# Kernel tuning notes

Measured on AMD Instinct MI355X. Metric: run time of the kernel, lower is better.

## Reference

```python
import jax, jax.numpy as jnp
import numpy as np
import math

N = 40000
E = 1280000
HID = 128
NF = 128
NG = 50
L = 3
CUTOFF = 10.0


def ssp(x):
    # shifted softplus: softplus(x) - log(2)
    return jax.nn.softplus(x) - jnp.float32(math.log(2.0))


def setup_inputs() -> dict:
    key = jax.random.key(0)
    ks = jax.random.split(key, 16)
    z = jax.random.randint(ks[0], (N,), 0, 100)
    pos = jax.random.normal(ks[1], (N, 3), dtype=jnp.float32) * 3.0
    batch = jnp.zeros((N,), dtype=jnp.int32)
    edge_index = jax.random.randint(ks[2], (2, E), 0, N)
    s = 0.1
    emb = jax.random.normal(ks[3], (100, HID), dtype=jnp.float32) * s
    mlp_w1 = jax.random.normal(ks[4], (L, NG, NF), dtype=jnp.float32) * s
    mlp_b1 = jnp.zeros((L, NF), dtype=jnp.float32)
    mlp_w2 = jax.random.normal(ks[5], (L, NF, NF), dtype=jnp.float32) * s
    mlp_b2 = jnp.zeros((L, NF), dtype=jnp.float32)
    conv_w1 = jax.random.normal(ks[6], (L, HID, NF), dtype=jnp.float32) * s  # no bias
    conv_w2 = jax.random.normal(ks[7], (L, NF, HID), dtype=jnp.float32) * s
    conv_b2 = jnp.zeros((L, HID), dtype=jnp.float32)
    lin_w = jax.random.normal(ks[8], (L, HID, HID), dtype=jnp.float32) * s
    lin_b = jnp.zeros((L, HID), dtype=jnp.float32)
    lin1_w = jax.random.normal(ks[9], (HID, HID // 2), dtype=jnp.float32) * s
    lin1_b = jnp.zeros((HID // 2,), dtype=jnp.float32)
    return {
        "z": z, "pos": pos, "batch": batch, "edge_index": edge_index,
        "emb": emb, "mlp_w1": mlp_w1, "mlp_b1": mlp_b1, "mlp_w2": mlp_w2,
        "mlp_b2": mlp_b2, "conv_w1": conv_w1, "conv_w2": conv_w2,
        "conv_b2": conv_b2, "lin_w": lin_w, "lin_b": lin_b,
        "lin1_w": lin1_w, "lin1_b": lin1_b,
    }


def reference(z, pos, batch, edge_index, emb, mlp_w1, mlp_b1, mlp_w2, mlp_b2,
              conv_w1, conv_w2, conv_b2, lin_w, lin_b, lin1_w, lin1_b):
    n = z.shape[0]
    row, col = edge_index[0], edge_index[1]
    # edge distances (radius-graph edge weights)
    diff = pos[row] - pos[col]                       # [E,3]
    edge_weight = jnp.sqrt(jnp.sum(diff * diff, axis=-1))  # [E]
    # Gaussian smearing
    offset = jnp.linspace(0.0, CUTOFF, NG, dtype=jnp.float32)
    coeff = -0.5 / (offset[1] - offset[0]) ** 2
    edge_attr = jnp.exp(coeff * (edge_weight[:, None] - offset[None, :]) ** 2)  # [E,NG]
    # cosine cutoff
    C = 0.5 * (jnp.cos(edge_weight * (jnp.pi / CUTOFF)) + 1.0)  # [E]

    h = emb[z]  # [N,HID]
    for l in range(L):
        W = ssp(edge_attr @ mlp_w1[l] + mlp_b1[l]) @ mlp_w2[l] + mlp_b2[l]  # [E,NF]
        W = W * C[:, None]
        x = h @ conv_w1[l]                      # [N,NF]
        msg = x[row] * W                        # gather + filter, [E,NF]
        agg = jax.ops.segment_sum(msg, col, num_segments=n)  # scatter-add, [N,NF]
        x = agg @ conv_w2[l] + conv_b2[l]       # [N,HID]
        x = ssp(x)
        x = x @ lin_w[l] + lin_b[l]
        h = h + x
    return ssp(h @ lin1_w + lin1_b)  # [N,HID//2]
```

## Files before the change

### kernel.cpp

```cpp
#include <hip/hip_runtime.h>
#include <math.h>


typedef _Float16 f16;
typedef _Float16 half8 __attribute__((ext_vector_type(8)));
typedef _Float16 half4v __attribute__((ext_vector_type(4)));
typedef float f32x4 __attribute__((ext_vector_type(4)));

#define NGAUSS 50
#define HIDF   128
#define NBINS  8192
#define DMAXF  40.0f
#define NLAYER 3
#define XST    132
#define BSHIFT 9
#define MAXBUCK 128
#define SCAP  20480

static __device__ __forceinline__ float sspf(float v) {
    return fmaxf(v, 0.0f) + log1pf(expf(-fabsf(v))) - 0.6931471805599453f;
}

__global__ __launch_bounds__(256) void k_stage(const int* __restrict__ ei,
                                               const float* __restrict__ pos,
                                               int* __restrict__ scnt,
                                               uint2* __restrict__ staging,
                                               int E, int nbuck) {
    const float SCALE = (float)(NBINS - 1) / DMAXF;
    __shared__ int bhist[MAXBUCK];
    __shared__ int boff[MAXBUCK];
    __shared__ int gpos[MAXBUCK];
    __shared__ uint2 recs[4096];
    __shared__ unsigned char lbuck[4096];
    int t = threadIdx.x;
    for (int i = t; i < nbuck; i += 256) bhist[i] = 0;
    __syncthreads();
    int e0 = blockIdx.x * 4096;
    int cnt_here = min(4096, E - e0);
    unsigned pay[16];
    unsigned short cc[16];
    short rk[16];
#pragma unroll
    for (int k = 0; k < 16; ++k) {
        int idx = t + k * 256;
        rk[k] = -1;
        if (idx < cnt_here) {
            int e = e0 + idx;
            int r = ei[e], c = ei[E + e];
            float dx = pos[3*r+0] - pos[3*c+0];
            float dy = pos[3*r+1] - pos[3*c+1];
            float dz = pos[3*r+2] - pos[3*c+2];
            float d = sqrtf(dx*dx + dy*dy + dz*dz);
            float u = fminf(d * SCALE, (float)(NBINS - 1));
            int i0 = min((int)u, NBINS - 2);
            float w0 = u - (float)i0;
            int wq = (int)(w0 * 8.0f + 0.5f);
            if (wq == 8) { i0 = min(i0 + 1, NBINS - 2); wq = 0; }
            pay[k] = ((unsigned)i0 << 19) | ((unsigned)wq << 16) | (unsigned)r;
            cc[k] = (unsigned short)c;
            rk[k] = (short)atomicAdd(&bhist[c >> BSHIFT], 1);
        }
    }
    __syncthreads();
    if (t == 0) {
        int run = 0;
        for (int b = 0; b < nbuck; ++b) { boff[b] = run; run += bhist[b]; }
    }
    __syncthreads();
    if (t < nbuck) gpos[t] = atomicAdd(&scnt[t], bhist[t]);
    __syncthreads();
#pragma unroll
    for (int k = 0; k < 16; ++k) {
        if (rk[k] >= 0) {
            int b = cc[k] >> BSHIFT;
            int slot = boff[b] + rk[k];
            recs[slot] = make_uint2(pay[k], (unsigned)cc[k]);
            lbuck[slot] = (unsigned char)b;
        }
    }
    __syncthreads();
    for (int i = t; i < cnt_here; i += 256) {
        int b = lbuck[i];
        staging[(size_t)b * SCAP + gpos[b] + (i - boff[b])] = recs[i];
    }
}

__global__ __launch_bounds__(1024) void k_place(const uint2* __restrict__ staging,
                                                const int* __restrict__ scnt,
                                                int* __restrict__ meta,
                                                int* __restrict__ offs,
                                                int n, int nbuck) {
    __shared__ int lcnt[512], loff[512], lcur[512];
    __shared__ int ldsm[SCAP];
    __shared__ int ebase_s;
    int b = blockIdx.x, t = threadIdx.x;
    int cntb = scnt[b];
    if (t == 0) {
        int run = 0;
        for (int j = 0; j < b; ++j) run += scnt[j];
        ebase_s = run;
    }
    for (int j = t; j < 512; j += 1024) { lcnt[j] = 0; lcur[j] = 0; }
    __syncthreads();
    int ebase = ebase_s;
    const uint2* sb = staging + (size_t)b * SCAP;
    for (int i = t; i < cntb; i += 1024)
        atomicAdd(&lcnt[sb[i].y & 511], 1);
    __syncthreads();
    if (t < 512) loff[t] = lcnt[t];
    __syncthreads();
    for (int o = 1; o < 512; o <<= 1) {
        int v = 0;
        if (t < 512) { v = loff[t]; if (t >= o) v += loff[t - o]; }
        __syncthreads();
        if (t < 512) loff[t] = v;
        __syncthreads();
    }
    int nb0 = b << BSHIFT;
    if (t < 512) {
        int node = nb0 + t;
        if (node < n) offs[node] = ebase + loff[t] - lcnt[t];
    }
    if (b == nbuck - 1 && t == 0) offs[n] = ebase + cntb;
    __syncthreads();
    for (int i = t; i < cntb; i += 1024) {
        uint2 r = sb[i];
        int cl = (int)(r.y & 511);
        int lpos = (loff[cl] - lcnt[cl]) + atomicAdd(&lcur[cl], 1);
        if (lpos < SCAP) ldsm[lpos] = (int)r.x;
        else meta[ebase + lpos] = (int)r.x;
    }
    __syncthreads();
    int lim = min(cntb, SCAP);
    for (int i = t; i < lim; i += 1024) meta[ebase + i] = ldsm[i];
}

__global__ __launch_bounds__(128) void k_table(const float* __restrict__ w1,
                                               const float* __restrict__ b1,
                                               const float* __restrict__ w2,
                                               const float* __restrict__ b2,
                                               f16* __restrict__ T) {
    const float DELTA = 10.0f / 49.0f;
    const float COEFF = -0.5f / (DELTA * DELTA);
    const float HSTEP = DMAXF / (float)(NBINS - 1);
    __shared__ float ea[8][NGAUSS];
    __shared__ float u[8][HIDF];
    int l = blockIdx.y, b0 = blockIdx.x * 8, j = threadIdx.x;
    for (int idx = j; idx < 8 * NGAUSS; idx += 128) {
        int bb = idx / NGAUSS, g = idx % NGAUSS;
        float d = (float)(b0 + bb) * HSTEP;
        float diff = d - (float)g * DELTA;
        ea[bb][g] = expf(COEFF * diff * diff);
    }
    __syncthreads();
    float acc[8];
    {
        float bias = b1[l * HIDF + j];
#pragma unroll
        for (int b = 0; b < 8; ++b) acc[b] = bias;
        const float* w1l = w1 + (size_t)l * NGAUSS * HIDF;
        for (int g = 0; g < NGAUSS; ++g) {
            float wv = w1l[g * HIDF + j];
#pragma unroll
            for (int b = 0; b < 8; ++b) acc[b] = fmaf(ea[b][g], wv, acc[b]);
        }
#pragma unroll
        for (int b = 0; b < 8; ++b) u[b][j] = sspf(acc[b]);
    }
    __syncthreads();
    {
        float bias = b2[l * HIDF + j];
#pragma unroll
        for (int b = 0; b < 8; ++b) acc[b] = bias;
        const float* w2l = w2 + (size_t)l * HIDF * HIDF;
        for (int k = 0; k < HIDF; ++k) {
            float wv = w2l[k * HIDF + j];
#pragma unroll
            for (int b = 0; b < 8; ++b) acc[b] = fmaf(u[b][k], wv, acc[b]);
        }
    }
    f16* Tl = T + ((size_t)l * NBINS + b0) * HIDF;
#pragma unroll
    for (int b = 0; b < 8; ++b) {
        float d = (float)(b0 + b) * HSTEP;
        float C = 0.5f * (cosf(d * (float)(M_PI / 10.0)) + 1.0f);
        Tl[b * HIDF + j] = (f16)(acc[b] * C);
    }
}

__global__ void k_wpack(const float* __restrict__ cw1, const float* __restrict__ cw2,
                        const float* __restrict__ lw, const float* __restrict__ l1w,
                        f16* __restrict__ Wp) {
    int mat = blockIdx.y;
    int N = (mat == 9) ? 64 : HIDF;
    int ntiles = N >> 4;
    int tid = blockIdx.x * 256 + threadIdx.x;
    int lane = tid & 63, ks = (tid >> 6) & 3, nt = tid >> 8;
    if (nt >= ntiles) return;
    const float* W;
    if (mat < 9) {
        int l = mat / 3, kind = mat % 3;
        W = (kind == 0 ? cw1 : kind == 1 ? cw2 : lw) + (size_t)l * HIDF * HIDF;
    } else {
        W = l1w;
    }
    int kbase = ks * 32 + (lane >> 4) * 8;
    int col = nt * 16 + (lane & 15);
    half8 st;
#pragma unroll
    for (int j = 0; j < 8; ++j) st[j] = (f16)W[(size_t)(kbase + j) * N + col];
    *(half8*)&Wp[(size_t)mat * 16384 + ((size_t)(nt * 4 + ks) * 64 + lane) * 8] = st;
}

#define AGG_EDGE(yy)                                                         \
    {                                                                        \
        int row_ = (yy) & 0xFFFF;                                            \
        int i0_ = ((unsigned)(yy)) >> 19;                                    \
        float w0_ = (float)(((yy) >> 16) & 7) * 0.125f;                      \
        half8 x0_ = *(const half8*)&xj[(size_t)row_ * HIDF];                 \
        half8 ta_ = *(const half8*)&Tj[(size_t)i0_ * HIDF];                  \
        half8 tb_ = *(const half8*)&Tj[(size_t)(i0_ + 1) * HIDF];            \
        _Pragma("unroll")                                                    \
        for (int j = 0; j < 8; ++j) {                                        \
            float t0 = (float)ta_[j];                                        \
            float f0 = fmaf(w0_, (float)tb_[j] - t0, t0);                    \
            a[j] = fmaf((float)x0_[j], f0, a[j]);                            \
        }                                                                    \
    }

__global__ __launch_bounds__(256) void k_agg(const f16* __restrict__ x,
                                             const f16* __restrict__ T,
                                             const int* __restrict__ meta,
                                             const int* __restrict__ offs,
                                             f16* __restrict__ agg, int n) {
    int node = (blockIdx.x * blockDim.x + threadIdx.x) >> 4;
    int lane = threadIdx.x & 15;
    if (node >= n) return;
    int beg = offs[node], end = offs[node + 1];
    const f16* xj = x + lane * 8;
    const f16* Tj = T + lane * 8;
    float a[8] = {};
    for (int chunk = beg; chunk < end; chunk += 16) {
        int cnt = min(16, end - chunk);
        int mm = meta[chunk + min(lane, cnt - 1)];
        int q = 0;
        for (; q + 4 <= cnt; q += 4) {
            int y0 = __shfl(mm, q + 0, 16);
            int y1 = __shfl(mm, q + 1, 16);
            int y2 = __shfl(mm, q + 2, 16);
            int y3 = __shfl(mm, q + 3, 16);
            AGG_EDGE(y0)
            AGG_EDGE(y1)
            AGG_EDGE(y2)
            AGG_EDGE(y3)
        }
        for (; q < cnt; ++q) {
            int y0 = __shfl(mm, q, 16);
            AGG_EDGE(y0)
        }
    }
    half8 st;
#pragma unroll
    for (int j = 0; j < 8; ++j) st[j] = (f16)a[j];
    *(half8*)&agg[(size_t)node * HIDF + lane * 8] = st;
}

__global__ __launch_bounds__(256) void k_init_gemm(const int* __restrict__ z,
                                                   const float* __restrict__ emb,
                                                   const f16* __restrict__ w1p,
                                                   f16* __restrict__ xout) {
    int lane = threadIdx.x & 63;
    int wid = threadIdx.x >> 6;
    int m0 = blockIdx.x * 64 + wid * 16;
    int mrow = lane & 15, quad = lane >> 4;
    const float* er = emb + (size_t)z[m0 + mrow] * HIDF + quad * 8;
    half8 afr[4];
#pragma unroll
    for (int ks = 0; ks < 4; ++ks) {
        float4 a = *(const float4*)(er + ks * 32);
        float4 b = *(const float4*)(er + ks * 32 + 4);
        half8 f = {(f16)a.x, (f16)a.y, (f16)a.z, (f16)a.w,
                   (f16)b.x, (f16)b.y, (f16)b.z, (f16)b.w};
        afr[ks] = f;
    }
    f32x4 acc[8];
#pragma unroll
    for (int t = 0; t < 8; ++t) acc[t] = (f32x4){0.f, 0.f, 0.f, 0.f};
    const f16* bp = w1p + (size_t)lane * 8;
#pragma unroll
    for (int t = 0; t < 8; ++t)
#pragma unroll
        for (int ks = 0; ks < 4; ++ks) {
            half8 bfr = *(const half8*)(bp + (size_t)(t * 4 + ks) * 512);
            acc[t] = __builtin_amdgcn_mfma_f32_16x16x32_f16(afr[ks], bfr, acc[t], 0, 0, 0);
        }
    int col0 = lane & 15;
    int growb = m0 + quad * 4;
#pragma unroll
    for (int t = 0; t < 8; ++t)
#pragma unroll
        for (int r = 0; r < 4; ++r)
            xout[(size_t)(growb + r) * HIDF + t * 16 + col0] = (f16)acc[t][r];
}

template <int NT3, bool LAYER0, bool WRITE_H>
__global__ __launch_bounds__(256) void k_fused(const f16* __restrict__ agg,
                                               const f16* __restrict__ w2p,
                                               const float* __restrict__ b2,
                                               const f16* __restrict__ lwp,
                                               const float* __restrict__ lb,
                                               const f16* __restrict__ b3p,
                                               const float* __restrict__ b3,
                                               float* __restrict__ hio,
                                               const int* __restrict__ z,
                                               const float* __restrict__ emb,
                                               f16* __restrict__ xout,
                                               float* __restrict__ fout) {
    __shared__ f16 Xs[4][16][XST];
    int lane = threadIdx.x & 63;
    int wid = threadIdx.x >> 6;
    int m0 = blockIdx.x * 64 + wid * 16;
    int mrow = lane & 15, quad = lane >> 4;
    int col0 = mrow;
    int growb = m0 + quad * 4;
    f16 (*X)[XST] = Xs[wid];

    half8 afr[4];
    {
        const f16* Ar = agg + (size_t)(m0 + mrow) * HIDF + quad * 8;
#pragma unroll
        for (int ks = 0; ks < 4; ++ks) afr[ks] = *(const half8*)(Ar + ks * 32);
    }
    f32x4 acc[8];
#pragma unroll
    for (int t = 0; t < 8; ++t) acc[t] = (f32x4){0.f, 0.f, 0.f, 0.f};
    {
        const f16* bp = w2p + (size_t)lane * 8;
#pragma unroll
        for (int t = 0; t < 8; ++t)
#pragma unroll
            for (int ks = 0; ks < 4; ++ks) {
                half8 bfr = *(const half8*)(bp + (size_t)(t * 4 + ks) * 512);
                acc[t] = __builtin_amdgcn_mfma_f32_16x16x32_f16(afr[ks], bfr, acc[t], 0, 0, 0);
            }
    }
#pragma unroll
    for (int t = 0; t < 8; ++t) {
        int col = t * 16 + col0;
        float bv = b2[col];
#pragma unroll
        for (int r = 0; r < 4; ++r)
            X[quad * 4 + r][col] = (f16)sspf(acc[t][r] + bv);
    }
#pragma unroll
    for (int ks = 0; ks < 4; ++ks) {
        half4v lo = *(const half4v*)&X[mrow][ks * 32 + quad * 8];
        half4v hi = *(const half4v*)&X[mrow][ks * 32 + quad * 8 + 4];
        half8 f;
#pragma unroll
        for (int j = 0; j < 4; ++j) { f[j] = lo[j]; f[4 + j] = hi[j]; }
        afr[ks] = f;
    }
#pragma unroll
    for (int t = 0; t < 8; ++t) acc[t] = (f32x4){0.f, 0.f, 0.f, 0.f};
    {
        const f16* bp = lwp + (size_t)lane * 8;
#pragma unroll
        for (int t = 0; t < 8; ++t)
#pragma unroll
            for (int ks = 0; ks < 4; ++ks) {
                half8 bfr = *(const half8*)(bp + (size_t)(t * 4 + ks) * 512);
                acc[t] = __builtin_amdgcn_mfma_f32_16x16x32_f16(afr[ks], bfr, acc[t], 0, 0, 0);
            }
    }
    int zr[4];
    if (LAYER0) {
#pragma unroll
        for (int r = 0; r < 4; ++r) zr[r] = z[growb + r];
    }
#pragma unroll
    for (int t = 0; t < 8; ++t) {
        int col = t * 16 + col0;
        float bv = lb[col];
#pragma unroll
        for (int r = 0; r < 4; ++r) {
            int grow = growb + r;
            float resid = LAYER0 ? emb[(size_t)zr[r] * HIDF + col]
                                 : hio[(size_t)grow * HIDF + col];
            float hp = acc[t][r] + bv + resid;
            if (WRITE_H) hio[(size_t)grow * HIDF + col] = hp;
            X[quad * 4 + r][col] = (f16)hp;
        }
    }
#pragma unroll
    for (int ks = 0; ks < 4; ++ks) {
        half4v lo = *(const half4v*)&X[mrow][ks * 32 + quad * 8];
        half4v hi = *(const half4v*)&X[mrow][ks * 32 + quad * 8 + 4];
        half8 f;
#pragma unroll
        for (int j = 0; j < 4; ++j) { f[j] = lo[j]; f[4 + j] = hi[j]; }
        afr[ks] = f;
    }
#pragma unroll
    for (int t = 0; t < NT3; ++t) acc[t] = (f32x4){0.f, 0.f, 0.f, 0.f};
    {
        const f16* bp = b3p + (size_t)lane * 8;
#pragma unroll
        for (int t = 0; t < NT3; ++t)
#pragma unroll
            for (int ks = 0; ks < 4; ++ks) {
                half8 bfr = *(const half8*)(bp + (size_t)(t * 4 + ks) * 512);
                acc[t] = __builtin_amdgcn_mfma_f32_16x16x32_f16(afr[ks], bfr, acc[t], 0, 0, 0);
            }
    }
    if (NT3 == 8) {
#pragma unroll
        for (int t = 0; t < 8; ++t)
#pragma unroll
            for (int r = 0; r < 4; ++r)
                xout[(size_t)(growb + r) * HIDF + t * 16 + col0] = (f16)acc[t][r];
    } else {
#pragma unroll
        for (int t = 0; t < NT3; ++t) {
            int col = t * 16 + col0;
            float bv = b3[col];
#pragma unroll
            for (int r = 0; r < 4; ++r)
                fout[(size_t)(growb + r) * (NT3 * 16) + col] = sspf(acc[t][r] + bv);
        }
    }
}

extern "C" void kernel_launch(void* const* d_in, const int* in_sizes, int n_in,
                              void* d_out, int out_size, void* d_ws, size_t ws_size,
                              hipStream_t stream) {
    const int*   z       = (const int*)d_in[0];
    const float* pos     = (const float*)d_in[1];
    const int*   ei      = (const int*)d_in[3];
    const float* emb     = (const float*)d_in[4];
    const float* mlp_w1  = (const float*)d_in[5];
    const float* mlp_b1  = (const float*)d_in[6];
    const float* mlp_w2  = (const float*)d_in[7];
    const float* mlp_b2  = (const float*)d_in[8];
    const float* conv_w1 = (const float*)d_in[9];
    const float* conv_w2 = (const float*)d_in[10];
    const float* conv_b2 = (const float*)d_in[11];
    const float* lin_w   = (const float*)d_in[12];
    const float* lin_b   = (const float*)d_in[13];
    const float* lin1_w  = (const float*)d_in[14];
    const float* lin1_b  = (const float*)d_in[15];
    float* out = (float*)d_out;

    int n = in_sizes[0];
    int E = in_sizes[3] / 2;
    int nbuck = (n + 511) >> 9;

    char* ws = (char*)d_ws;
    size_t off = 0;
    auto alloc = [&](size_t bytes) -> void* {
        void* p = ws + off;
        off = (off + bytes + 255) & ~(size_t)255;
        return p;
    };
    float* h     = (float*)alloc((size_t)n * HIDF * 4);
    f16*   x16   = (f16*)alloc((size_t)n * HIDF * 2);
    f16*   agg16 = (f16*)alloc((size_t)n * HIDF * 2);
    f16*   T16   = (f16*)alloc((size_t)NLAYER * NBINS * HIDF * 2);
    int*   meta  = (int*)alloc((size_t)E * 4);
    int*   offs  = (int*)alloc((size_t)(n + 1) * 4);
    int*   scnt  = (int*)alloc((size_t)nbuck * 4);
    uint2* staging = (uint2*)alloc((size_t)nbuck * SCAP * 8);
    f16*   Wp    = (f16*)alloc((size_t)10 * 16384 * 2);

    const int tb = 256;
    hipMemsetAsync(scnt, 0, (size_t)nbuck * 4, stream);
    hipLaunchKernelGGL(k_stage, dim3((E + 4095) / 4096), dim3(tb), 0, stream,
                       ei, pos, scnt, staging, E, nbuck);
    hipLaunchKernelGGL(k_place, dim3(nbuck), dim3(1024), 0, stream,
                       staging, scnt, meta, offs, n, nbuck);
    hipLaunchKernelGGL(k_wpack, dim3(8, 10), dim3(tb), 0, stream,
                       conv_w1, conv_w2, lin_w, lin1_w, Wp);
    hipLaunchKernelGGL(k_table, dim3(NBINS / 8, NLAYER), dim3(128), 0, stream,
                       mlp_w1, mlp_b1, mlp_w2, mlp_b2, T16);

    int gemmblocks = n / 64;
    int aggblocks = (n * 16 + tb - 1) / tb;
    hipLaunchKernelGGL(k_init_gemm, dim3(gemmblocks), dim3(tb), 0, stream,
                       z, emb, Wp + (size_t)0 * 16384, x16);
    hipLaunchKernelGGL(k_agg, dim3(aggblocks), dim3(tb), 0, stream,
                       x16, T16 + (size_t)0 * NBINS * HIDF, meta, offs, agg16, n);
    hipLaunchKernelGGL(HIP_KERNEL_NAME(k_fused<8, true, true>), dim3(gemmblocks), dim3(tb), 0, stream,
                       agg16, Wp + (size_t)1 * 16384, conv_b2 + 0 * HIDF,
                       Wp + (size_t)2 * 16384, lin_b + 0 * HIDF,
                       Wp + (size_t)3 * 16384, (const float*)nullptr,
                       h, z, emb, x16, (float*)nullptr);
    hipLaunchKernelGGL(k_agg, dim3(aggblocks), dim3(tb), 0, stream,
                       x16, T16 + (size_t)1 * NBINS * HIDF, meta, offs, agg16, n);
    hipLaunchKernelGGL(HIP_KERNEL_NAME(k_fused<8, false, true>), dim3(gemmblocks), dim3(tb), 0, stream,
                       agg16, Wp + (size_t)4 * 16384, conv_b2 + 1 * HIDF,
                       Wp + (size_t)5 * 16384, lin_b + 1 * HIDF,
                       Wp + (size_t)6 * 16384, (const float*)nullptr,
                       h, (const int*)nullptr, (const float*)nullptr, x16, (float*)nullptr);
    hipLaunchKernelGGL(k_agg, dim3(aggblocks), dim3(tb), 0, stream,
                       x16, T16 + (size_t)2 * NBINS * HIDF, meta, offs, agg16, n);
    hipLaunchKernelGGL(HIP_KERNEL_NAME(k_fused<4, false, false>), dim3(gemmblocks), dim3(tb), 0, stream,
                       agg16, Wp + (size_t)7 * 16384, conv_b2 + 2 * HIDF,
                       Wp + (size_t)8 * 16384, lin_b + 2 * HIDF,
                       Wp + (size_t)9 * 16384, lin1_b,
                       h, (const int*)nullptr, (const float*)nullptr, (f16*)nullptr, out);
    (void)n_in; (void)out_size; (void)ws_size;
}
```

Baseline: 439.2 us.

## Shrink CSR buckets, parallelize scans, use packed fp16 interpolation in aggregation

Bucket size for the counting-sort CSR build drops from 512 to 128 nodes, so there are more, smaller buckets and k_place runs more blocks with less LDS. The serial prefix sums over bucket counts in k_stage and k_place become wavefront shuffle scans. The aggregation kernel now does the filter-table interpolation with packed half8 arithmetic and uses nontemporal loads and stores for meta and agg. The fp16 interpolation lowers accuracy slightly, and the extra buckets increase global atomics on scnt.

Measured after the change: 471.8 us. +7.4%, slower.

```diff
diff --git a/kernel.cpp b/kernel.cpp
--- a/kernel.cpp
+++ b/kernel.cpp
@@ -13,9 +13,10 @@
 #define DMAXF  40.0f
 #define NLAYER 3
 #define XST    132
-#define BSHIFT 9
-#define MAXBUCK 128
-#define SCAP  20480
+#define BSHIFT 7
+#define NPB    128
+#define MAXBUCK 512
+#define SCAP  5120
 
 static __device__ __forceinline__ float sspf(float v) {
     return fmaxf(v, 0.0f) + log1pf(expf(-fabsf(v))) - 0.6931471805599453f;
@@ -31,9 +32,9 @@
     __shared__ int boff[MAXBUCK];
     __shared__ int gpos[MAXBUCK];
     __shared__ uint2 recs[4096];
-    __shared__ unsigned char lbuck[4096];
+    __shared__ unsigned short lbuck[4096];
     int t = threadIdx.x;
-    for (int i = t; i < nbuck; i += 256) bhist[i] = 0;
+    for (int i = t; i < MAXBUCK; i += 256) bhist[i] = 0;
     __syncthreads();
     int e0 = blockIdx.x * 4096;
     int cnt_here = min(4096, E - e0);
@@ -62,20 +63,30 @@
         }
     }
     __syncthreads();
-    if (t == 0) {
+    if (t < 64) {
+        int base = t * 8;
+        int s[8];
         int run = 0;
-        for (int b = 0; b < nbuck; ++b) { boff[b] = run; run += bhist[b]; }
-    }
-    __syncthreads();
-    if (t < nbuck) gpos[t] = atomicAdd(&scnt[t], bhist[t]);
-    __syncthreads();
+#pragma unroll
+        for (int j = 0; j < 8; ++j) { s[j] = run; run += bhist[base + j]; }
+        int incl = run;
+        for (int o = 1; o < 64; o <<= 1) {
+            int v = __shfl_up(incl, o, 64);
+            if (t >= o) incl += v;
+        }
+        int excl = incl - run;
+#pragma unroll
+        for (int j = 0; j < 8; ++j) boff[base + j] = excl + s[j];
+    }
+    __syncthreads();
+    for (int i = t; i < nbuck; i += 256) gpos[i] = atomicAdd(&scnt[i], bhist[i]);
 #pragma unroll
     for (int k = 0; k < 16; ++k) {
         if (rk[k] >= 0) {
             int b = cc[k] >> BSHIFT;
             int slot = boff[b] + rk[k];
             recs[slot] = make_uint2(pay[k], (unsigned)cc[k]);
-            lbuck[slot] = (unsigned char)b;
+            lbuck[slot] = (unsigned short)b;
         }
     }
     __syncthreads();
@@ -90,34 +101,39 @@
                                                 int* __restrict__ meta,
                                                 int* __restrict__ offs,
                                                 int n, int nbuck) {
-    __shared__ int lcnt[512], loff[512], lcur[512];
+    __shared__ int lcnt[NPB], loff[NPB], lcur[NPB];
     __shared__ int ldsm[SCAP];
+    __shared__ int wsum[16];
     __shared__ int ebase_s;
     int b = blockIdx.x, t = threadIdx.x;
     int cntb = scnt[b];
+    int part = 0;
+    for (int j = t; j < b; j += 1024) part += scnt[j];
+    for (int o = 32; o > 0; o >>= 1) part += __shfl_down(part, o, 64);
+    if ((t & 63) == 0) wsum[t >> 6] = part;
+    if (t < NPB) { lcnt[t] = 0; lcur[t] = 0; }
+    __syncthreads();
     if (t == 0) {
-        int run = 0;
-        for (int j = 0; j < b; ++j) run += scnt[j];
-        ebase_s = run;
-    }
-    for (int j = t; j < 512; j += 1024) { lcnt[j] = 0; lcur[j] = 0; }
-    __syncthreads();
-    int ebase = ebase_s;
+        int r = 0;
+        for (int w = 0; w < 16; ++w) r += wsum[w];
+        ebase_s = r;
+    }
     const uint2* sb = staging + (size_t)b * SCAP;
     for (int i = t; i < cntb; i += 1024)
-        atomicAdd(&lcnt[sb[i].y & 511], 1);
-    __syncthreads();
-    if (t < 512) loff[t] = lcnt[t];
-    __syncthreads();
-    for (int o = 1; o < 512; o <<= 1) {
+        atomicAdd(&lcnt[sb[i].y & (NPB - 1)], 1);
+    __syncthreads();
+    int ebase = ebase_s;
+    if (t < NPB) loff[t] = lcnt[t];
+    __syncthreads();
+    for (int o = 1; o < NPB; o <<= 1) {
         int v = 0;
-        if (t < 512) { v = loff[t]; if (t >= o) v += loff[t - o]; }
+        if (t < NPB) { v = loff[t]; if (t >= o) v += loff[t - o]; }
         __syncthreads();
-        if (t < 512) loff[t] = v;
+        if (t < NPB) loff[t] = v;
         __syncthreads();
     }
     int nb0 = b << BSHIFT;
-    if (t < 512) {
+    if (t < NPB) {
         int node = nb0 + t;
         if (node < n) offs[node] = ebase + loff[t] - lcnt[t];
     }
@@ -125,7 +141,7 @@
     __syncthreads();
     for (int i = t; i < cntb; i += 1024) {
         uint2 r = sb[i];
-        int cl = (int)(r.y & 511);
+        int cl = (int)(r.y & (NPB - 1));
         int lpos = (loff[cl] - lcnt[cl]) + atomicAdd(&lcur[cl], 1);
         if (lpos < SCAP) ldsm[lpos] = (int)r.x;
         else meta[ebase + lpos] = (int)r.x;
@@ -216,16 +232,17 @@
     {                                                                        \
         int row_ = (yy) & 0xFFFF;                                            \
         int i0_ = ((unsigned)(yy)) >> 19;                                    \
-        float w0_ = (float)(((yy) >> 16) & 7) * 0.125f;                      \
+        f16 w0h_ = (f16)((float)(((yy) >> 16) & 7) * 0.125f);                \
         half8 x0_ = *(const half8*)&xj[(size_t)row_ * HIDF];                 \
         half8 ta_ = *(const half8*)&Tj[(size_t)i0_ * HIDF];                  \
         half8 tb_ = *(const half8*)&Tj[(size_t)(i0_ + 1) * HIDF];            \
+        half8 w0v_;                                                          \
         _Pragma("unroll")                                                    \
-        for (int j = 0; j < 8; ++j) {                                        \
-            float t0 = (float)ta_[j];                                        \
-            float f0 = fmaf(w0_, (float)tb_[j] - t0, t0);                    \
-            a[j] = fmaf((float)x0_[j], f0, a[j]);                            \
-        }                                                                    \
+        for (int j = 0; j < 8; ++j) w0v_[j] = w0h_;                          \
+        half8 f_ = ta_ + w0v_ * (tb_ - ta_);                                 \
+        _Pragma("unroll")                                                    \
+        for (int j = 0; j < 8; ++j)                                          \
+            a[j] = fmaf((float)x0_[j], (float)f_[j], a[j]);                  \
     }
 
 __global__ __launch_bounds__(256) void k_agg(const f16* __restrict__ x,
@@ -242,7 +259,7 @@
     float a[8] = {};
     for (int chunk = beg; chunk < end; chunk += 16) {
         int cnt = min(16, end - chunk);
-        int mm = meta[chunk + min(lane, cnt - 1)];
+        int mm = __builtin_nontemporal_load(&meta[chunk + min(lane, cnt - 1)]);
         int q = 0;
         for (; q + 4 <= cnt; q += 4) {
             int y0 = __shfl(mm, q + 0, 16);
@@ -262,7 +279,7 @@
     half8 st;
 #pragma unroll
     for (int j = 0; j < 8; ++j) st[j] = (f16)a[j];
-    *(half8*)&agg[(size_t)node * HIDF + lane * 8] = st;
+    __builtin_nontemporal_store(st, (half8*)&agg[(size_t)node * HIDF + lane * 8]);
 }
 
 __global__ __launch_bounds__(256) void k_init_gemm(const int* __restrict__ z,
@@ -453,7 +470,7 @@
 
     int n = in_sizes[0];
     int E = in_sizes[3] / 2;
-    int nbuck = (n + 511) >> 9;
+    int nbuck = (n + NPB - 1) >> BSHIFT;
 
     char* ws = (char*)d_ws;
     size_t off = 0;
```
